# Kernel optimization log

Hardware: AMD Instinct MI355X
Metric: run time of the kernel (lower is better)

Reference implementation:

```python
import jax, jax.numpy as jnp
import numpy as np

E = 64        # num_experts
K = 6         # num_experts_per_tok
D = 2048      # hidden_size
F = 1408      # moe_intermediate_size (per expert)
NSH = 2       # num_shared_experts
FS = F * NSH  # shared-expert intermediate
T = 2048      # tokens (batch*seq flattened)
CAP = 512     # expert capacity; mean load T*K/E=192, CAP is >20 sigma above -> no drops


def setup_inputs() -> dict:
    key = jax.random.key(0)
    ks = jax.random.split(key, 9)
    s = 0.02
    return {
        "hidden_states": jax.random.normal(ks[0], (T, D), jnp.float32),
        "gate_w": jax.random.normal(ks[1], (E, D), jnp.float32) * s,
        "w_gate": jax.random.normal(ks[2], (E, D, F), jnp.float32) * s,
        "w_up": jax.random.normal(ks[3], (E, D, F), jnp.float32) * s,
        "w_down": jax.random.normal(ks[4], (E, F, D), jnp.float32) * s,
        "ws_gate": jax.random.normal(ks[5], (D, FS), jnp.float32) * s,
        "ws_up": jax.random.normal(ks[6], (D, FS), jnp.float32) * s,
        "ws_down": jax.random.normal(ks[7], (FS, D), jnp.float32) * s,
    }


def reference(hidden_states, gate_w, w_gate, w_up, w_down, ws_gate, ws_up, ws_down):
    x = hidden_states  # [T, D]
    n_tok = x.shape[0]

    # ---- gate: softmax -> top-k -> renormalize (bailing_moe norm_topk_prob) ----
    probs = jax.nn.softmax(x @ gate_w.T, axis=-1)           # [T, E]
    topw, topi = jax.lax.top_k(probs, K)                    # [T, K]
    topw = topw / jnp.sum(topw, axis=-1, keepdims=True)

    flat_e = topi.reshape(-1)                               # [T*K] expert id per assignment
    flat_w = topw.reshape(-1)                               # [T*K] combine weight
    tok = jnp.arange(n_tok * K) // K                        # [T*K] source token (idxs // k)

    # ---- dispatch: slot of each assignment within its expert (== sort-by-expert) ----
    onehot = jax.nn.one_hot(flat_e, E, dtype=jnp.int32)     # [T*K, E]
    slot = jnp.take_along_axis(jnp.cumsum(onehot, axis=0) - onehot,
                               flat_e[:, None], axis=1)[:, 0]  # [T*K]
    valid = slot < CAP                                      # all True given CAP margin
    slot_c = jnp.where(valid, slot, CAP - 1)

    xa = x[tok] * valid[:, None].astype(x.dtype)            # [T*K, D] gathered tokens
    buf = jnp.zeros((E, CAP, D), x.dtype).at[flat_e, slot_c].add(xa)  # [E, CAP, D]

    # ---- per-expert SwiGLU MLP as grouped GEMMs ----
    h = jax.nn.silu(jnp.einsum('ecd,edf->ecf', buf, w_gate)) \
        * jnp.einsum('ecd,edf->ecf', buf, w_up)             # [E, CAP, F]
    o = jnp.einsum('ecf,efd->ecd', h, w_down)               # [E, CAP, D]

    # ---- combine: weighted scatter-add back to tokens ----
    ya = o[flat_e, slot_c] * (flat_w * valid.astype(flat_w.dtype))[:, None]
    y = jax.ops.segment_sum(ya, tok, num_segments=n_tok)    # [T, D]

    # ---- shared experts (SwiGLU on identity) ----
    shared = (jax.nn.silu(x @ ws_gate) * (x @ ws_up)) @ ws_down
    return y + shared
```

## Files before the change

kernel.cpp:

```cpp
#include <hip/hip_runtime.h>
#include <hip/hip_bf16.h>
#include <cstdint>

typedef __attribute__((ext_vector_type(4))) float f4;
typedef __attribute__((ext_vector_type(4))) float f32x4;
typedef __attribute__((ext_vector_type(8))) __bf16 bf16x8;
typedef unsigned short ushort_t;
typedef unsigned int uint_t;

#define TTOK 2048
#define DDIM 2048
#define NEXP 64
#define TOPK 6
#define FDIM 1408
#define FSH  2816
#define NASSIGN (TTOK*TOPK)

__device__ __forceinline__ ushort_t f2bf(float f){
  uint_t u = __builtin_bit_cast(uint_t, f);
  u = (u + 0x7FFFu + ((u >> 16) & 1u)) >> 16;
  return (ushort_t)u;
}
__device__ __forceinline__ float bf2f(uint_t b){
  uint_t u = (b & 0xFFFFu) << 16;
  return __builtin_bit_cast(float, u);
}
__device__ __forceinline__ void gld_lds16(const void* g, void* l){
  __builtin_amdgcn_global_load_lds((const __attribute__((address_space(1))) uint_t*)g,
                                   (__attribute__((address_space(3))) uint_t*)l, 16, 0, 0);
}

__global__ __launch_bounds__(256) void gate_topk_kernel(
    const float* __restrict__ x, const float* __restrict__ gw,
    int* __restrict__ topi, float* __restrict__ topw)
{
  __shared__ float xs[4*2048];
  __shared__ float lg[4*64];
  int tid = threadIdx.x;
  int t0 = blockIdx.x*4;
  const f4* xg = (const f4*)(x + (size_t)t0*DDIM);
  f4* xsv = (f4*)xs;
  for (int i = tid; i < 2048; i += 256) xsv[i] = xg[i];
  __syncthreads();
  int g = tid >> 6, l = tid & 63;
  int c = l & 3, er = l >> 2;
  const f4* xrow = (const f4*)(xs + g*2048 + c*512);
  #pragma unroll
  for (int eo = 0; eo < 4; ++eo){
    int e = eo*16 + er;
    const f4* wrow = (const f4*)(gw + (size_t)e*DDIM + c*512);
    float d = 0.f;
    #pragma unroll 4
    for (int j = 0; j < 128; ++j){
      f4 w = wrow[j], a = xrow[j];
      d += w.x*a.x + w.y*a.y + w.z*a.z + w.w*a.w;
    }
    d += __shfl_xor(d, 1);
    d += __shfl_xor(d, 2);
    if (c == 0) lg[g*64 + e] = d;
  }
  __syncthreads();
  float mv = lg[g*64 + l];
  float sv[6]; int si[6];
  #pragma unroll
  for (int s = 0; s < 6; ++s){
    float bv = mv; int bi = l;
    for (int off = 32; off > 0; off >>= 1){
      float ov = __shfl_xor(bv, off);
      int oi = __shfl_xor(bi, off);
      if (ov > bv || (ov == bv && oi < bi)){ bv = ov; bi = oi; }
    }
    sv[s] = bv; si[s] = bi;
    if (l == bi) mv = -3.4e38f;
  }
  if (l == 0){
    float sum = 0.f, wv[6];
    #pragma unroll
    for (int s = 0; s < 6; ++s){ wv[s] = __expf(sv[s] - sv[0]); sum += wv[s]; }
    float inv = 1.f/sum;
    int t = t0 + g;
    #pragma unroll
    for (int s = 0; s < 6; ++s){ topi[t*6+s] = si[s]; topw[t*6+s] = wv[s]*inv; }
  }
}

__global__ __launch_bounds__(256) void xcast_kernel(const float* __restrict__ x, ushort_t* __restrict__ xb){
  size_t base = ((size_t)blockIdx.x*256 + threadIdx.x)*8;
  f4 a = *(const f4*)(x + base);
  f4 b = *(const f4*)(x + base + 4);
  uint4 r;
  r.x = f2bf(a.x) | ((uint_t)f2bf(a.y)<<16);
  r.y = f2bf(a.z) | ((uint_t)f2bf(a.w)<<16);
  r.z = f2bf(b.x) | ((uint_t)f2bf(b.y)<<16);
  r.w = f2bf(b.z) | ((uint_t)f2bf(b.w)<<16);
  *(uint4*)(xb + base) = r;
}

__global__ __launch_bounds__(256) void count_kernel(const int* __restrict__ topi, int* __restrict__ counts){
  int a = blockIdx.x*256 + threadIdx.x;
  if (a < NASSIGN) atomicAdd(&counts[topi[a]], 1);
}
__global__ void scan_kernel(const int* __restrict__ counts, int* __restrict__ offsets){
  if (threadIdx.x == 0){
    int s = 0;
    for (int e = 0; e < NEXP; ++e){ offsets[e] = s; s += counts[e]; }
    offsets[NEXP] = s;
  }
}
__global__ __launch_bounds__(256) void scatter_kernel(
    const int* __restrict__ topi, const float* __restrict__ topw,
    const int* __restrict__ offsets, int* __restrict__ cursor,
    int* __restrict__ row_token, float* __restrict__ row_w, int* __restrict__ row_assign)
{
  int a = blockIdx.x*256 + threadIdx.x;
  if (a < NASSIGN){
    int e = topi[a];
    int pos = atomicAdd(&cursor[e], 1);
    int r = offsets[e] + pos;
    row_token[r]  = a / 6;
    row_w[r]      = topw[a];
    row_assign[r] = a;
  }
}

__global__ __launch_bounds__(512, 2) void gemm_gateup_kernel(
    const ushort_t* __restrict__ A, const float* __restrict__ Bg0, const float* __restrict__ Bu0,
    ushort_t* __restrict__ H,
    const int* __restrict__ offsets, const int* __restrict__ row_token,
    const ushort_t* __restrict__ zerop,
    int N, int K, int lda, int n_mt, int n_nt, int Mfix)
{
  int nwg = gridDim.x;
  int chunk = nwg >> 3;
  int L = (blockIdx.x & 7)*chunk + (blockIdx.x >> 3);
  int e, mt, nt, row0, rowcnt;
  if (offsets){
    int per = n_mt*n_nt; e = L/per; int rem = L - e*per; mt = rem/n_nt; nt = rem - mt*n_nt;
    row0 = offsets[e]; rowcnt = offsets[e+1] - row0;
  } else { e = 0; nt = L/n_mt; mt = L - nt*n_mt; row0 = 0; rowcnt = Mfix; }
  int m0 = mt*256;
  if (m0 >= rowcnt) return;

  const float* Bg = Bg0 + (size_t)e*K*N + nt*64;
  const float* Bu = Bu0 + (size_t)e*K*N + nt*64;

  __shared__ ushort_t As[256*64];
  __shared__ ushort_t Bs[2][64*64];

  int tid = threadIdx.x;
  int lane = tid & 63;
  int wid = tid >> 6;
  int wm = wid & 3, wn = wid >> 2;

  const ushort_t* asrc[4];
  #pragma unroll
  for (int i = 0; i < 4; ++i){
    int r = (tid >> 3) + i*64;
    int gr = m0 + r;
    bool v = gr < rowcnt;
    int tok = row_token ? (v ? row_token[row0+gr] : 0) : gr;
    const ushort_t* p = v ? (A + (size_t)tok*lda) : zerop;
    int slot = (tid & 7) ^ (r & 7);
    asrc[i] = p + slot*8;
  }

  int half = tid >> 8;
  int l256 = tid & 255;
  int bn4 = l256 & 15, bk4 = l256 >> 4;
  const float* Bsrc = half ? Bu : Bg;
  ushort_t* bdst[4];
  #pragma unroll
  for (int j = 0; j < 4; ++j){
    int n = bn4*4 + j;
    int slot = (bk4 >> 1) ^ (n & 7);
    bdst[j] = &Bs[half][n*64 + slot*8 + (bk4 & 1)*4];
  }

  f32x4 accG[4][2], accU[4][2];
  #pragma unroll
  for (int i=0;i<4;++i)
    #pragma unroll
    for (int j=0;j<2;++j){ accG[i][j] = f32x4{0.f,0.f,0.f,0.f}; accU[i][j] = f32x4{0.f,0.f,0.f,0.f}; }

  int nK = K >> 6;
  for (int ks = 0; ks < nK; ++ks){
    int k0 = ks << 6;
    #pragma unroll
    for (int i = 0; i < 4; ++i)
      gld_lds16(asrc[i] + k0, &As[i*4096 + tid*8]);
    const float* bp = Bsrc + (size_t)(k0 + bk4*4)*N + bn4*4;
    f4 v0 = *(const f4*)(bp);
    f4 v1 = *(const f4*)(bp + (size_t)N);
    f4 v2 = *(const f4*)(bp + 2*(size_t)N);
    f4 v3 = *(const f4*)(bp + 3*(size_t)N);
    #pragma unroll
    for (int j = 0; j < 4; ++j){
      uint2 pk;
      pk.x = f2bf(v0[j]) | ((uint_t)f2bf(v1[j]) << 16);
      pk.y = f2bf(v2[j]) | ((uint_t)f2bf(v3[j]) << 16);
      *(uint2*)bdst[j] = pk;
    }
    __syncthreads();
    #pragma unroll
    for (int kk = 0; kk < 2; ++kk){
      bf16x8 af[4], bg[2], bu[2];
      int kb = (kk << 2) + (lane >> 4);
      #pragma unroll
      for (int i = 0; i < 4; ++i){
        int ar = wm*64 + i*16 + (lane & 15);
        af[i] = *(const bf16x8*)&As[ar*64 + ((kb ^ (ar & 7)) << 3)];
      }
      #pragma unroll
      for (int j = 0; j < 2; ++j){
        int br = wn*32 + j*16 + (lane & 15);
        int idx = br*64 + ((kb ^ (br & 7)) << 3);
        bg[j] = *(const bf16x8*)&Bs[0][idx];
        bu[j] = *(const bf16x8*)&Bs[1][idx];
      }
      #pragma unroll
      for (int i = 0; i < 4; ++i)
        #pragma unroll
        for (int j = 0; j < 2; ++j){
          accG[i][j] = __builtin_amdgcn_mfma_f32_16x16x32_bf16(af[i], bg[j], accG[i][j], 0,0,0);
          accU[i][j] = __builtin_amdgcn_mfma_f32_16x16x32_bf16(af[i], bu[j], accU[i][j], 0,0,0);
        }
    }
    __syncthreads();
  }

  #pragma unroll
  for (int i = 0; i < 4; ++i)
    #pragma unroll
    for (int j = 0; j < 2; ++j){
      int col = nt*64 + wn*32 + j*16 + (lane & 15);
      #pragma unroll
      for (int q = 0; q < 4; ++q){
        int r = wm*64 + i*16 + ((lane >> 4) << 2) + q;
        int gr = m0 + r;
        if (gr < rowcnt){
          float gv = accG[i][j][q];
          float uv = accU[i][j][q];
          float hv = (gv / (1.f + __expf(-gv))) * uv;
          H[(size_t)(row0 + gr)*(size_t)N + col] = f2bf(hv);
        }
      }
    }
}

__global__ __launch_bounds__(512, 2) void gemm_down_kernel(
    const ushort_t* __restrict__ A, const float* __restrict__ B0,
    ushort_t* __restrict__ outb, float* __restrict__ outf,
    const int* __restrict__ offsets, const float* __restrict__ row_w, const int* __restrict__ row_assign,
    const ushort_t* __restrict__ zerop,
    int N, int K, int lda, int n_mt, int n_nt, int Mfix)
{
  int nwg = gridDim.x;
  int chunk = nwg >> 3;
  int L = (blockIdx.x & 7)*chunk + (blockIdx.x >> 3);
  int e, mt, nt, row0, rowcnt;
  if (offsets){
    int per = n_mt*n_nt; e = L/per; int rem = L - e*per; mt = rem/n_nt; nt = rem - mt*n_nt;
    row0 = offsets[e]; rowcnt = offsets[e+1] - row0;
  } else { e = 0; nt = L/n_mt; mt = L - nt*n_mt; row0 = 0; rowcnt = Mfix; }
  int m0 = mt*256;
  if (m0 >= rowcnt) return;

  const float* B = B0 + (size_t)e*K*N + nt*64;

  __shared__ ushort_t As[256*64];
  __shared__ ushort_t Bs[64*64];
  __shared__ float Wr[256];
  __shared__ int Ar[256];

  int tid = threadIdx.x;
  int lane = tid & 63;
  int wid = tid >> 6;
  int wm = wid & 3, wn = wid >> 2;

  if (offsets){
    for (int t = tid; t < 256; t += 512){
      int gr = m0 + t;
      bool v = gr < rowcnt;
      Wr[t] = v ? row_w[row0+gr] : 0.f;
      Ar[t] = v ? row_assign[row0+gr] : 0;
    }
  }

  const ushort_t* asrc[4];
  #pragma unroll
  for (int i = 0; i < 4; ++i){
    int r = (tid >> 3) + i*64;
    int gr = m0 + r;
    bool v = gr < rowcnt;
    const ushort_t* p = v ? (A + (size_t)(row0+gr)*lda) : zerop;
    int slot = (tid & 7) ^ (r & 7);
    asrc[i] = p + slot*8;
  }

  int bn4 = tid & 15, bk8 = tid >> 4;
  ushort_t* bdst[4];
  #pragma unroll
  for (int j = 0; j < 4; ++j){
    int n = bn4*4 + j;
    int slot = (bk8 >> 2) ^ (n & 7);
    bdst[j] = &Bs[n*64 + slot*8 + (bk8 & 3)*2];
  }

  f32x4 acc[4][2];
  #pragma unroll
  for (int i=0;i<4;++i)
    #pragma unroll
    for (int j=0;j<2;++j) acc[i][j] = f32x4{0.f,0.f,0.f,0.f};

  int nK = K >> 6;
  for (int ks = 0; ks < nK; ++ks){
    int k0 = ks << 6;
    #pragma unroll
    for (int i = 0; i < 4; ++i)
      gld_lds16(asrc[i] + k0, &As[i*4096 + tid*8]);
    const float* bp = B + (size_t)(k0 + bk8*2)*N + bn4*4;
    f4 v0 = *(const f4*)(bp);
    f4 v1 = *(const f4*)(bp + (size_t)N);
    #pragma unroll
    for (int j = 0; j < 4; ++j){
      uint_t pk = f2bf(v0[j]) | ((uint_t)f2bf(v1[j]) << 16);
      *(uint_t*)bdst[j] = pk;
    }
    __syncthreads();
    #pragma unroll
    for (int kk = 0; kk < 2; ++kk){
      bf16x8 af[4], bb[2];
      int kb = (kk << 2) + (lane >> 4);
      #pragma unroll
      for (int i = 0; i < 4; ++i){
        int ar = wm*64 + i*16 + (lane & 15);
        af[i] = *(const bf16x8*)&As[ar*64 + ((kb ^ (ar & 7)) << 3)];
      }
      #pragma unroll
      for (int j = 0; j < 2; ++j){
        int br = wn*32 + j*16 + (lane & 15);
        bb[j] = *(const bf16x8*)&Bs[br*64 + ((kb ^ (br & 7)) << 3)];
      }
      #pragma unroll
      for (int i = 0; i < 4; ++i)
        #pragma unroll
        for (int j = 0; j < 2; ++j)
          acc[i][j] = __builtin_amdgcn_mfma_f32_16x16x32_bf16(af[i], bb[j], acc[i][j], 0,0,0);
    }
    __syncthreads();
  }

  #pragma unroll
  for (int i = 0; i < 4; ++i)
    #pragma unroll
    for (int j = 0; j < 2; ++j){
      int col = nt*64 + wn*32 + j*16 + (lane & 15);
      #pragma unroll
      for (int q = 0; q < 4; ++q){
        int r = wm*64 + i*16 + ((lane >> 4) << 2) + q;
        int gr = m0 + r;
        if (gr < rowcnt){
          float val = acc[i][j][q];
          if (offsets){
            outb[(size_t)Ar[r]*2048 + col] = f2bf(val * Wr[r]);
          } else {
            outf[(size_t)gr*2048 + col] = val;
          }
        }
      }
    }
}

__global__ __launch_bounds__(256) void combine_kernel(const ushort_t* __restrict__ oa, float* __restrict__ out){
  size_t base = ((size_t)blockIdx.x*256 + threadIdx.x)*8;
  int t = (int)(base >> 11);
  int d = (int)(base & 2047);
  f4 s0 = *(const f4*)(out + base);
  f4 s1 = *(const f4*)(out + base + 4);
  #pragma unroll
  for (int k = 0; k < 6; ++k){
    const ushort_t* row = oa + (((size_t)(t*6+k)) << 11) + d;
    uint4 u = *(const uint4*)row;
    s0.x += bf2f(u.x); s0.y += bf2f(u.x >> 16);
    s0.z += bf2f(u.y); s0.w += bf2f(u.y >> 16);
    s1.x += bf2f(u.z); s1.y += bf2f(u.z >> 16);
    s1.z += bf2f(u.w); s1.w += bf2f(u.w >> 16);
  }
  *(f4*)(out + base) = s0;
  *(f4*)(out + base + 4) = s1;
}

extern "C" void kernel_launch(void* const* d_in, const int* in_sizes, int n_in,
                              void* d_out, int out_size, void* d_ws, size_t ws_size,
                              hipStream_t stream)
{
  const float* x       = (const float*)d_in[0];
  const float* gate_w  = (const float*)d_in[1];
  const float* w_gate  = (const float*)d_in[2];
  const float* w_up    = (const float*)d_in[3];
  const float* w_down  = (const float*)d_in[4];
  const float* ws_gate = (const float*)d_in[5];
  const float* ws_up   = (const float*)d_in[6];
  const float* ws_down = (const float*)d_in[7];
  float* out = (float*)d_out;

  char* ws = (char*)d_ws;
  int*      topi       = (int*)(ws + 0);
  float*    topw       = (float*)(ws + 49152);
  int*      counts     = (int*)(ws + 98304);
  int*      cursor     = (int*)(ws + 98560);
  int*      offsets    = (int*)(ws + 98816);
  int*      row_token  = (int*)(ws + 99328);
  float*    row_w      = (float*)(ws + 148480);
  int*      row_assign = (int*)(ws + 197632);
  ushort_t* zerop      = (ushort_t*)(ws + 262144);
  ushort_t* xb         = (ushort_t*)(ws + 524288);
  ushort_t* Hbuf       = (ushort_t*)(ws + 8912896);
  ushort_t* Shbuf      = (ushort_t*)(ws + 43515904);
  ushort_t* oa         = (ushort_t*)(ws + 55050240);
  (void)ws_size; (void)in_sizes; (void)n_in; (void)out_size;

  hipMemsetAsync(ws + 98304, 0, 512, stream);
  hipMemsetAsync(zerop, 0, 8192, stream);

  gate_topk_kernel<<<512, 256, 0, stream>>>(x, gate_w, topi, topw);
  xcast_kernel<<<2048, 256, 0, stream>>>(x, xb);
  count_kernel<<<48, 256, 0, stream>>>(topi, counts);
  scan_kernel<<<1, 64, 0, stream>>>(counts, offsets);
  scatter_kernel<<<48, 256, 0, stream>>>(topi, topw, offsets, cursor, row_token, row_w, row_assign);

  gemm_gateup_kernel<<<2816, 512, 0, stream>>>(xb, w_gate, w_up, Hbuf, offsets, row_token, zerop,
                                               FDIM, DDIM, DDIM, 2, 22, 0);
  gemm_gateup_kernel<<<352, 512, 0, stream>>>(xb, ws_gate, ws_up, Shbuf, nullptr, nullptr, zerop,
                                              FSH, DDIM, DDIM, 8, 44, TTOK);
  gemm_down_kernel<<<256, 512, 0, stream>>>(Shbuf, ws_down, nullptr, out, nullptr, nullptr, nullptr, zerop,
                                            DDIM, FSH, FSH, 8, 32, TTOK);
  gemm_down_kernel<<<4096, 512, 0, stream>>>(Hbuf, w_down, oa, nullptr, offsets, row_w, row_assign, zerop,
                                             DDIM, FDIM, FDIM, 2, 32, 0);
  combine_kernel<<<2048, 256, 0, stream>>>(oa, out);
}
```

Baseline: 959.6 us.

## Double-buffer LDS tiles in gate/up and down GEMMs to overlap loads with MFMA

Adds two-stage LDS buffering to both grouped GEMM kernels. The next K-tile's A rows (direct global-to-LDS loads) and fp32 B values are fetched before the current tile's MFMAs, and B is converted to bf16 and stored into the other buffer afterwards, so only one barrier per iteration remains. This hides global memory latency behind compute but doubles LDS use (gate/up goes to about 64KB) and keeps prefetched registers live. The down kernel's launch bound also rises from 2 to 4 blocks per CU, which tightens the register budget.

```diff
diff --git a/kernel.cpp b/kernel.cpp
--- a/kernel.cpp
+++ b/kernel.cpp
@@ -144,8 +144,8 @@
   const float* Bg = Bg0 + (size_t)e*K*N + nt*64;
   const float* Bu = Bu0 + (size_t)e*K*N + nt*64;
 
-  __shared__ ushort_t As[256*64];
-  __shared__ ushort_t Bs[2][64*64];
+  __shared__ ushort_t As[2][256*64];
+  __shared__ ushort_t Bs[2][2*64*64];
 
   int tid = threadIdx.x;
   int lane = tid & 63;
@@ -168,12 +168,12 @@
   int l256 = tid & 255;
   int bn4 = l256 & 15, bk4 = l256 >> 4;
   const float* Bsrc = half ? Bu : Bg;
-  ushort_t* bdst[4];
+  int bdoff[4];
   #pragma unroll
   for (int j = 0; j < 4; ++j){
     int n = bn4*4 + j;
     int slot = (bk4 >> 1) ^ (n & 7);
-    bdst[j] = &Bs[half][n*64 + slot*8 + (bk4 & 1)*4];
+    bdoff[j] = half*4096 + n*64 + slot*8 + (bk4 & 1)*4;
   }
 
   f32x4 accG[4][2], accU[4][2];
@@ -183,12 +183,11 @@
     for (int j=0;j<2;++j){ accG[i][j] = f32x4{0.f,0.f,0.f,0.f}; accU[i][j] = f32x4{0.f,0.f,0.f,0.f}; }
 
   int nK = K >> 6;
-  for (int ks = 0; ks < nK; ++ks){
-    int k0 = ks << 6;
-    #pragma unroll
-    for (int i = 0; i < 4; ++i)
-      gld_lds16(asrc[i] + k0, &As[i*4096 + tid*8]);
-    const float* bp = Bsrc + (size_t)(k0 + bk4*4)*N + bn4*4;
+  #pragma unroll
+  for (int i = 0; i < 4; ++i)
+    gld_lds16(asrc[i], &As[0][i*4096 + tid*8]);
+  {
+    const float* bp = Bsrc + (size_t)(bk4*4)*N + bn4*4;
     f4 v0 = *(const f4*)(bp);
     f4 v1 = *(const f4*)(bp + (size_t)N);
     f4 v2 = *(const f4*)(bp + 2*(size_t)N);
@@ -198,9 +197,28 @@
       uint2 pk;
       pk.x = f2bf(v0[j]) | ((uint_t)f2bf(v1[j]) << 16);
       pk.y = f2bf(v2[j]) | ((uint_t)f2bf(v3[j]) << 16);
-      *(uint2*)bdst[j] = pk;
-    }
-    __syncthreads();
+      *(uint2*)&Bs[0][bdoff[j]] = pk;
+    }
+  }
+  __syncthreads();
+
+  for (int ks = 0; ks < nK; ++ks){
+    int cur = ks & 1, nxt = cur ^ 1;
+    bool pf = (ks + 1) < nK;
+    if (pf){
+      int k0n = (ks + 1) << 6;
+      #pragma unroll
+      for (int i = 0; i < 4; ++i)
+        gld_lds16(asrc[i] + k0n, &As[nxt][i*4096 + tid*8]);
+    }
+    f4 v0, v1, v2, v3;
+    if (pf){
+      const float* bp = Bsrc + (size_t)(((ks + 1) << 6) + bk4*4)*N + bn4*4;
+      v0 = *(const f4*)(bp);
+      v1 = *(const f4*)(bp + (size_t)N);
+      v2 = *(const f4*)(bp + 2*(size_t)N);
+      v3 = *(const f4*)(bp + 3*(size_t)N);
+    }
     #pragma unroll
     for (int kk = 0; kk < 2; ++kk){
       bf16x8 af[4], bg[2], bu[2];
@@ -208,14 +226,14 @@
       #pragma unroll
       for (int i = 0; i < 4; ++i){
         int ar = wm*64 + i*16 + (lane & 15);
-        af[i] = *(const bf16x8*)&As[ar*64 + ((kb ^ (ar & 7)) << 3)];
+        af[i] = *(const bf16x8*)&As[cur][ar*64 + ((kb ^ (ar & 7)) << 3)];
       }
       #pragma unroll
       for (int j = 0; j < 2; ++j){
         int br = wn*32 + j*16 + (lane & 15);
         int idx = br*64 + ((kb ^ (br & 7)) << 3);
-        bg[j] = *(const bf16x8*)&Bs[0][idx];
-        bu[j] = *(const bf16x8*)&Bs[1][idx];
+        bg[j] = *(const bf16x8*)&Bs[cur][idx];
+        bu[j] = *(const bf16x8*)&Bs[cur][4096 + idx];
       }
       #pragma unroll
       for (int i = 0; i < 4; ++i)
@@ -224,6 +242,15 @@
           accG[i][j] = __builtin_amdgcn_mfma_f32_16x16x32_bf16(af[i], bg[j], accG[i][j], 0,0,0);
           accU[i][j] = __builtin_amdgcn_mfma_f32_16x16x32_bf16(af[i], bu[j], accU[i][j], 0,0,0);
         }
+    }
+    if (pf){
+      #pragma unroll
+      for (int j = 0; j < 4; ++j){
+        uint2 pk;
+        pk.x = f2bf(v0[j]) | ((uint_t)f2bf(v1[j]) << 16);
+        pk.y = f2bf(v2[j]) | ((uint_t)f2bf(v3[j]) << 16);
+        *(uint2*)&Bs[nxt][bdoff[j]] = pk;
+      }
     }
     __syncthreads();
   }
@@ -247,7 +274,7 @@
     }
 }
 
-__global__ __launch_bounds__(512, 2) void gemm_down_kernel(
+__global__ __launch_bounds__(512, 4) void gemm_down_kernel(
     const ushort_t* __restrict__ A, const float* __restrict__ B0,
     ushort_t* __restrict__ outb, float* __restrict__ outf,
     const int* __restrict__ offsets, const float* __restrict__ row_w, const int* __restrict__ row_assign,
@@ -267,8 +294,8 @@
 
   const float* B = B0 + (size_t)e*K*N + nt*64;
 
-  __shared__ ushort_t As[256*64];
-  __shared__ ushort_t Bs[64*64];
+  __shared__ ushort_t As[2][256*64];
+  __shared__ ushort_t Bs[2][64*64];
   __shared__ float Wr[256];
   __shared__ int Ar[256];
 
@@ -298,12 +325,12 @@
   }
 
   int bn4 = tid & 15, bk8 = tid >> 4;
-  ushort_t* bdst[4];
+  int bdoff[4];
   #pragma unroll
   for (int j = 0; j < 4; ++j){
     int n = bn4*4 + j;
     int slot = (bk8 >> 2) ^ (n & 7);
-    bdst[j] = &Bs[n*64 + slot*8 + (bk8 & 3)*2];
+    bdoff[j] = n*64 + slot*8 + (bk8 & 3)*2;
   }
 
   f32x4 acc[4][2];
@@ -313,20 +340,36 @@
     for (int j=0;j<2;++j) acc[i][j] = f32x4{0.f,0.f,0.f,0.f};
 
   int nK = K >> 6;
-  for (int ks = 0; ks < nK; ++ks){
-    int k0 = ks << 6;
-    #pragma unroll
-    for (int i = 0; i < 4; ++i)
-      gld_lds16(asrc[i] + k0, &As[i*4096 + tid*8]);
-    const float* bp = B + (size_t)(k0 + bk8*2)*N + bn4*4;
+  #pragma unroll
+  for (int i = 0; i < 4; ++i)
+    gld_lds16(asrc[i], &As[0][i*4096 + tid*8]);
+  {
+    const float* bp = B + (size_t)(bk8*2)*N + bn4*4;
     f4 v0 = *(const f4*)(bp);
     f4 v1 = *(const f4*)(bp + (size_t)N);
     #pragma unroll
     for (int j = 0; j < 4; ++j){
       uint_t pk = f2bf(v0[j]) | ((uint_t)f2bf(v1[j]) << 16);
-      *(uint_t*)bdst[j] = pk;
-    }
-    __syncthreads();
+      *(uint_t*)&Bs[0][bdoff[j]] = pk;
+    }
+  }
+  __syncthreads();
+
+  for (int ks = 0; ks < nK; ++ks){
+    int cur = ks & 1, nxt = cur ^ 1;
+    bool pf = (ks + 1) < nK;
+    if (pf){
+      int k0n = (ks + 1) << 6;
+      #pragma unroll
+      for (int i = 0; i < 4; ++i)
+        gld_lds16(asrc[i] + k0n, &As[nxt][i*4096 + tid*8]);
+    }
+    f4 v0, v1;
+    if (pf){
+      const float* bp = B + (size_t)(((ks + 1) << 6) + bk8*2)*N + bn4*4;
+      v0 = *(const f4*)(bp);
+      v1 = *(const f4*)(bp + (size_t)N);
+    }
     #pragma unroll
     for (int kk = 0; kk < 2; ++kk){
       bf16x8 af[4], bb[2];
@@ -334,18 +377,25 @@
       #pragma unroll
       for (int i = 0; i < 4; ++i){
         int ar = wm*64 + i*16 + (lane & 15);
-        af[i] = *(const bf16x8*)&As[ar*64 + ((kb ^ (ar & 7)) << 3)];
+        af[i] = *(const bf16x8*)&As[cur][ar*64 + ((kb ^ (ar & 7)) << 3)];
       }
       #pragma unroll
       for (int j = 0; j < 2; ++j){
         int br = wn*32 + j*16 + (lane & 15);
-        bb[j] = *(const bf16x8*)&Bs[br*64 + ((kb ^ (br & 7)) << 3)];
+        bb[j] = *(const bf16x8*)&Bs[cur][br*64 + ((kb ^ (br & 7)) << 3)];
       }
       #pragma unroll
       for (int i = 0; i < 4; ++i)
         #pragma unroll
         for (int j = 0; j < 2; ++j)
           acc[i][j] = __builtin_amdgcn_mfma_f32_16x16x32_bf16(af[i], bb[j], acc[i][j], 0,0,0);
+    }
+    if (pf){
+      #pragma unroll
+      for (int j = 0; j < 4; ++j){
+        uint_t pk = f2bf(v0[j]) | ((uint_t)f2bf(v1[j]) << 16);
+        *(uint_t*)&Bs[nxt][bdoff[j]] = pk;
+      }
     }
     __syncthreads();
   }
```

After: 1.135 ms. 1.18x slower.
